# Optimization experiments

Hardware: AMD Instinct MI355X
Metric: run time of the kernel (lower is better)

The kernel has to match this reference:

```python
import jax, jax.numpy as jnp
import numpy as np

B, S, D, H = 4, 2048, 1024, 16
HD = D // H


def setup_inputs() -> dict:
    key = jax.random.key(0)
    ks = jax.random.split(key, 5)
    scale = 0.02
    return {
        "x": jax.random.normal(ks[0], (B, S, D), dtype=jnp.float32),
        "Wq": jax.random.normal(ks[1], (D, D), dtype=jnp.float32) * scale,
        "Wk": jax.random.normal(ks[2], (D, D), dtype=jnp.float32) * scale,
        "Wv": jax.random.normal(ks[3], (D, D), dtype=jnp.float32) * scale,
        "Wo": jax.random.normal(ks[4], (D, D), dtype=jnp.float32) * scale,
    }


def reference(x, Wq, Wk, Wv, Wo):
    b, s, d = x.shape
    # Linear layers (torch Linear: y = x @ W.T), no bias
    q = jnp.einsum('bsd,ed->bse', x, Wq).reshape(b, s, H, HD).transpose(0, 2, 1, 3)
    k = jnp.einsum('bsd,ed->bse', x, Wk).reshape(b, s, H, HD).transpose(0, 2, 1, 3)
    v = jnp.einsum('bsd,ed->bse', x, Wv).reshape(b, s, H, HD).transpose(0, 2, 1, 3)
    # [B,H,S,S] attention scores
    scores = jnp.einsum('bhqd,bhkd->bhqk', q, k)
    causal = jnp.tril(jnp.ones((s, s), dtype=bool))
    scores = jnp.where(causal, scores, -jnp.inf)
    # faithful to source: mask first, then scale, then softmax
    weights = jax.nn.softmax(scores / jnp.sqrt(jnp.float32(HD)), axis=-1)
    # dropout p=0.0 (eval): identity
    ctx = jnp.einsum('bhqk,bhkd->bhqd', weights, v)
    ctx = ctx.transpose(0, 2, 1, 3).reshape(b, s, d)
    return jnp.einsum('bsd,ed->bse', ctx, Wo)
```

## Files before the change

### kernel.cpp

```cpp
#include <hip/hip_runtime.h>
#include <math.h>

typedef unsigned short u16;
typedef __attribute__((ext_vector_type(8))) short short8;
typedef __attribute__((ext_vector_type(4))) float f32x4;

constexpr int Bb = 4, S_LEN = 2048, DMODEL = 1024, NH = 16;
constexpr int MTOT = Bb * S_LEN;

__device__ __forceinline__ u16 f2bf(float f) {
    union { float f; unsigned u; } v; v.f = f;
    unsigned r = v.u + 0x7FFFu + ((v.u >> 16) & 1u);
    return (u16)(r >> 16);
}

__device__ __forceinline__ void load_lds16(const void* g, void* l) {
    __builtin_amdgcn_global_load_lds(
        (const __attribute__((address_space(1))) unsigned int*)g,
        (__attribute__((address_space(3))) unsigned int*)l, 16, 0, 0);
}

__global__ __launch_bounds__(256)
void cvt_all(const float* __restrict__ x,
             const float* __restrict__ w0, const float* __restrict__ w1,
             const float* __restrict__ w2, const float* __restrict__ w3,
             u16* __restrict__ xb, u16* __restrict__ b0, u16* __restrict__ b1,
             u16* __restrict__ b2, u16* __restrict__ b3)
{
    int gid = blockIdx.x * 256 + threadIdx.x;
    constexpr int NXo = (MTOT * DMODEL) / 8;
    constexpr int NWo = (DMODEL * DMODEL) / 8;
    const float* s; u16* d; int o;
    if (gid < NXo) { s = x; d = xb; o = gid; }
    else {
        int t = gid - NXo;
        int w = t >> 17;
        o = t & (NWo - 1);
        s = (w == 0) ? w0 : (w == 1) ? w1 : (w == 2) ? w2 : w3;
        d = (w == 0) ? b0 : (w == 1) ? b1 : (w == 2) ? b2 : b3;
    }
    const float4* sp = (const float4*)(s + (size_t)o * 8);
    float4 a = sp[0], bq = sp[1];
    short8 ov;
    ov[0] = (short)f2bf(a.x);  ov[1] = (short)f2bf(a.y);
    ov[2] = (short)f2bf(a.z);  ov[3] = (short)f2bf(a.w);
    ov[4] = (short)f2bf(bq.x); ov[5] = (short)f2bf(bq.y);
    ov[6] = (short)f2bf(bq.z); ov[7] = (short)f2bf(bq.w);
    *(short8*)(d + (size_t)o * 8) = ov;
}

__global__ __launch_bounds__(256, 2)
void gemm_bt(const u16* __restrict__ X,
             const u16* __restrict__ W0, const u16* __restrict__ W1, const u16* __restrict__ W2,
             u16* __restrict__ Y0, u16* __restrict__ Y1, u16* __restrict__ Y2,
             int M, int N, int K)
{
    const u16* W = (blockIdx.z == 0) ? W0 : (blockIdx.z == 1) ? W1 : W2;
    u16*       Y = (blockIdx.z == 0) ? Y0 : (blockIdx.z == 1) ? Y1 : Y2;

    __shared__ __align__(16) u16 lA[128 * 64];
    __shared__ __align__(16) u16 lB[128 * 64];

    const int tid  = threadIdx.x;
    const int wave = tid >> 6;
    const int lane = tid & 63;
    const int qd   = lane >> 4;
    const int c    = lane & 15;
    const int tm   = blockIdx.x * 128;
    const int tn   = blockIdx.y * 128;
    const int wm   = (wave >> 1) * 64;
    const int wn   = (wave & 1) * 64;

    f32x4 acc[4][4] = {};

    for (int k0 = 0; k0 < K; k0 += 64) {
        if (k0) __syncthreads();
#pragma unroll
        for (int it = 0; it < 4; ++it) {
            int chunk = it * 256 + tid;
            int row = chunk >> 3, hc = chunk & 7;
            load_lds16(X + (size_t)(tm + row) * K + k0 + hc * 8,
                       (char*)lA + (it * 256 + wave * 64) * 16);
            load_lds16(W + (size_t)(tn + row) * K + k0 + hc * 8,
                       (char*)lB + (it * 256 + wave * 64) * 16);
        }
        __syncthreads();

#pragma unroll
        for (int kk = 0; kk < 64; kk += 32) {
            short8 a[4], b[4];
#pragma unroll
            for (int i = 0; i < 4; ++i) {
                a[i] = *(const short8*)&lA[(wm + i * 16 + c) * 64 + kk + qd * 8];
                b[i] = *(const short8*)&lB[(wn + i * 16 + c) * 64 + kk + qd * 8];
            }
#pragma unroll
            for (int mi = 0; mi < 4; ++mi)
#pragma unroll
                for (int ni = 0; ni < 4; ++ni)
                    acc[mi][ni] = __builtin_amdgcn_mfma_f32_16x16x32_bf16(
                        a[mi], b[ni], acc[mi][ni], 0, 0, 0);
        }
    }

#pragma unroll
    for (int mi = 0; mi < 4; ++mi)
#pragma unroll
        for (int ni = 0; ni < 4; ++ni)
#pragma unroll
            for (int r = 0; r < 4; ++r) {
                int row = tm + wm + mi * 16 + qd * 4 + r;
                int col = tn + wn + ni * 16 + c;
                Y[(size_t)row * N + col] = f2bf(acc[mi][ni][r]);
            }
}

__global__ __launch_bounds__(256, 2)
void gemm_bt_f32(const u16* __restrict__ X, const u16* __restrict__ W,
                 float* __restrict__ Y, int M, int N, int K)
{
    __shared__ __align__(16) u16 lA[128 * 64];
    __shared__ __align__(16) u16 lB[128 * 64];

    const int tid  = threadIdx.x;
    const int wave = tid >> 6;
    const int lane = tid & 63;
    const int qd   = lane >> 4;
    const int c    = lane & 15;
    const int tm   = blockIdx.x * 128;
    const int tn   = blockIdx.y * 128;
    const int wm   = (wave >> 1) * 64;
    const int wn   = (wave & 1) * 64;

    f32x4 acc[4][4] = {};

    for (int k0 = 0; k0 < K; k0 += 64) {
        if (k0) __syncthreads();
#pragma unroll
        for (int it = 0; it < 4; ++it) {
            int chunk = it * 256 + tid;
            int row = chunk >> 3, hc = chunk & 7;
            load_lds16(X + (size_t)(tm + row) * K + k0 + hc * 8,
                       (char*)lA + (it * 256 + wave * 64) * 16);
            load_lds16(W + (size_t)(tn + row) * K + k0 + hc * 8,
                       (char*)lB + (it * 256 + wave * 64) * 16);
        }
        __syncthreads();

#pragma unroll
        for (int kk = 0; kk < 64; kk += 32) {
            short8 a[4], b[4];
#pragma unroll
            for (int i = 0; i < 4; ++i) {
                a[i] = *(const short8*)&lA[(wm + i * 16 + c) * 64 + kk + qd * 8];
                b[i] = *(const short8*)&lB[(wn + i * 16 + c) * 64 + kk + qd * 8];
            }
#pragma unroll
            for (int mi = 0; mi < 4; ++mi)
#pragma unroll
                for (int ni = 0; ni < 4; ++ni)
                    acc[mi][ni] = __builtin_amdgcn_mfma_f32_16x16x32_bf16(
                        a[mi], b[ni], acc[mi][ni], 0, 0, 0);
        }
    }

#pragma unroll
    for (int mi = 0; mi < 4; ++mi)
#pragma unroll
        for (int ni = 0; ni < 4; ++ni)
#pragma unroll
            for (int r = 0; r < 4; ++r) {
                int row = tm + wm + mi * 16 + qd * 4 + r;
                int col = tn + wn + ni * 16 + c;
                Y[(size_t)row * N + col] = acc[mi][ni][r];
            }
}

__global__ __launch_bounds__(256)
void transpose_v(const u16* __restrict__ V, u16* __restrict__ VT)
{
    const int sblk = blockIdx.x;
    const int bh   = blockIdx.y;
    const int b = bh >> 4, h = bh & 15;
    __shared__ __align__(16) u16 lT[64][72];

    const int t = threadIdx.x;
#pragma unroll
    for (int it = 0; it < 2; ++it) {
        int chunk = it * 256 + t;
        int si = chunk >> 3, hc = chunk & 7;
        short8 val = *(const short8*)&V[(size_t)(b * S_LEN + sblk * 64 + si) * DMODEL + h * 64 + hc * 8];
        *(short8*)&lT[si][hc * 8] = val;
    }
    __syncthreads();
#pragma unroll
    for (int it = 0; it < 2; ++it) {
        int chunk = it * 256 + t;
        int hd = chunk >> 3, sc = chunk & 7;
        short8 o;
#pragma unroll
        for (int j = 0; j < 8; ++j) o[j] = (short)lT[sc * 8 + j][hd];
        *(short8*)&VT[(size_t)(bh * 64 + hd) * S_LEN + sblk * 64 + sc * 8] = o;
    }
}

__global__ __launch_bounds__(256, 2)
void attention(const u16* __restrict__ Q, const u16* __restrict__ K,
               const u16* __restrict__ VT, u16* __restrict__ CTX)
{
    const int p  = blockIdx.x;
    const int bh = blockIdx.y;
    const int b = bh >> 4, h = bh & 15;

    __shared__ __align__(16) u16 lK[2][64 * 64];
    __shared__ __align__(16) u16 lV[2][64 * 64];
    __shared__ __align__(16) u16 lP[128 * 72];

    const int tid = threadIdx.x, wave = tid >> 6, lane = tid & 63;
    const int qd = lane >> 4, c = lane & 15;
    const int wrow = wave * 32;
    const int srow = tid >> 3, shc = tid & 7;
    const int shcs = shc ^ (srow & 7);
    const int rx   = c & 7;
    const size_t kbase = (size_t)(b * S_LEN) * DMODEL + h * 64;
    const size_t vbase = (size_t)(bh * 64) * S_LEN;

#pragma unroll
    for (int phase = 0; phase < 2; ++phase) {
        const int qt = phase ? (15 - p) : p;
        const int q0 = qt * 128;
        const int nkv = 2 * qt + 2;

        short8 qf[2][2];
#pragma unroll
        for (int mi = 0; mi < 2; ++mi)
#pragma unroll
            for (int ks = 0; ks < 2; ++ks)
                qf[mi][ks] = *(const short8*)&Q[(size_t)(b * S_LEN + q0 + wrow + mi * 16 + c) * DMODEL
                                                + h * 64 + ks * 32 + qd * 8];

        f32x4 oacc[2][4] = {};
        float psum[2][4] = {};

        __syncthreads();
#pragma unroll
        for (int it = 0; it < 2; ++it) {
            load_lds16(K + kbase + (size_t)(it * 32 + srow) * DMODEL + shcs * 8,
                       (char*)lK[0] + (it * 256 + wave * 64) * 16);
            load_lds16(VT + vbase + (size_t)(it * 32 + srow) * S_LEN + shcs * 8,
                       (char*)lV[0] + (it * 256 + wave * 64) * 16);
        }

        for (int kt = 0; kt < nkv; ++kt) {
            const int cur = kt & 1;
            const int k0 = kt * 64;
            __syncthreads();

            if (kt + 1 < nkv) {
                const int kn = (kt + 1) * 64;
#pragma unroll
                for (int it = 0; it < 2; ++it) {
                    load_lds16(K + kbase + (size_t)(kn + it * 32 + srow) * DMODEL + shcs * 8,
                               (char*)lK[cur ^ 1] + (it * 256 + wave * 64) * 16);
                    load_lds16(VT + vbase + (size_t)(it * 32 + srow) * S_LEN + kn + shcs * 8,
                               (char*)lV[cur ^ 1] + (it * 256 + wave * 64) * 16);
                }
            }

            f32x4 sacc[2][4] = {};
#pragma unroll
            for (int ks = 0; ks < 2; ++ks) {
                short8 kf[4];
#pragma unroll
                for (int ni = 0; ni < 4; ++ni)
                    kf[ni] = *(const short8*)&lK[cur][(ni * 16 + c) * 64
                                                      + (((ks * 4 + qd) ^ rx) << 3)];
#pragma unroll
                for (int mi = 0; mi < 2; ++mi)
#pragma unroll
                    for (int ni = 0; ni < 4; ++ni)
                        sacc[mi][ni] = __builtin_amdgcn_mfma_f32_16x16x32_bf16(
                            qf[mi][ks], kf[ni], sacc[mi][ni], 0, 0, 0);
            }

            const bool need_mask = (k0 + 63 > q0);
#pragma unroll
            for (int mi = 0; mi < 2; ++mi)
#pragma unroll
                for (int ni = 0; ni < 4; ++ni)
#pragma unroll
                    for (int r = 0; r < 4; ++r) {
                        float t = sacc[mi][ni][r] * 0.125f;
                        if (need_mask) {
                            int colg = k0 + ni * 16 + c;
                            int rowg = q0 + wrow + mi * 16 + qd * 4 + r;
                            if (colg > rowg) t = -1.0e38f;
                        }
                        t = fminf(t, 60.0f);
                        float pv = __expf(t);
                        psum[mi][r] += pv;
                        lP[(wrow + mi * 16 + qd * 4 + r) * 72 + ni * 16 + c] = f2bf(pv);
                    }

            asm volatile("s_waitcnt lgkmcnt(0)" ::: "memory");

#pragma unroll
            for (int ks2 = 0; ks2 < 2; ++ks2) {
                short8 af[2], bf[4];
#pragma unroll
                for (int mi = 0; mi < 2; ++mi)
                    af[mi] = *(const short8*)&lP[(wrow + mi * 16 + c) * 72 + ks2 * 32 + qd * 8];
#pragma unroll
                for (int ni = 0; ni < 4; ++ni)
                    bf[ni] = *(const short8*)&lV[cur][(ni * 16 + c) * 64
                                                      + (((ks2 * 4 + qd) ^ rx) << 3)];
#pragma unroll
                for (int mi = 0; mi < 2; ++mi)
#pragma unroll
                    for (int ni = 0; ni < 4; ++ni)
                        oacc[mi][ni] = __builtin_amdgcn_mfma_f32_16x16x32_bf16(
                            af[mi], bf[ni], oacc[mi][ni], 0, 0, 0);
            }
        }

        float linv[2][4];
#pragma unroll
        for (int mi = 0; mi < 2; ++mi)
#pragma unroll
            for (int r = 0; r < 4; ++r) {
                float l = psum[mi][r];
#pragma unroll
                for (int d = 1; d < 16; d <<= 1) l += __shfl_xor(l, d);
                linv[mi][r] = 1.0f / l;
            }
#pragma unroll
        for (int mi = 0; mi < 2; ++mi)
#pragma unroll
            for (int ni = 0; ni < 4; ++ni)
#pragma unroll
                for (int r = 0; r < 4; ++r) {
                    int row = q0 + wrow + mi * 16 + qd * 4 + r;
                    CTX[(size_t)(b * S_LEN + row) * DMODEL + h * 64 + ni * 16 + c]
                        = f2bf(oacc[mi][ni][r] * linv[mi][r]);
                }
    }
}

extern "C" void kernel_launch(void* const* d_in, const int* in_sizes, int n_in,
                              void* d_out, int out_size, void* d_ws, size_t ws_size,
                              hipStream_t stream)
{
    const size_t MB = 1024 * 1024;
    char* ws = (char*)d_ws;
    if (ws_size < 72 * MB + 64) return;

    u16* xb  = (u16*)ws;
    u16* wb0 = (u16*)(ws + 16 * MB);
    u16* wb1 = (u16*)(ws + 18 * MB);
    u16* wb2 = (u16*)(ws + 20 * MB);
    u16* wb3 = (u16*)(ws + 22 * MB);
    u16* q   = (u16*)(ws + 24 * MB);
    u16* k   = (u16*)(ws + 40 * MB);
    u16* v   = (u16*)(ws + 56 * MB);
    u16* vt  = xb;
    u16* ctx = v;
    float* out = (float*)d_out;

    constexpr int NCVT = (MTOT * DMODEL + 4 * DMODEL * DMODEL) / 8 / 256;

    cvt_all<<<NCVT, 256, 0, stream>>>(
        (const float*)d_in[0], (const float*)d_in[1], (const float*)d_in[2],
        (const float*)d_in[3], (const float*)d_in[4], xb, wb0, wb1, wb2, wb3);

    gemm_bt<<<dim3(MTOT / 128, DMODEL / 128, 3), 256, 0, stream>>>(
        xb, wb0, wb1, wb2, q, k, v, MTOT, DMODEL, DMODEL);
    transpose_v<<<dim3(S_LEN / 64, Bb * NH), 256, 0, stream>>>(v, vt);
    attention<<<dim3(8, Bb * NH), 256, 0, stream>>>(q, k, vt, ctx);
    gemm_bt_f32<<<dim3(MTOT / 128, DMODEL / 128, 1), 256, 0, stream>>>(
        ctx, wb3, out, MTOT, DMODEL, DMODEL);
}
```

Before: 271.5 us.

## Split attention work across 8 waves with 16 query rows each

The attention kernel now launches 512 threads per block instead of 256, so each wave owns 16 query rows instead of 32. The K/V tile loads are spread across twice as many threads, halving each thread's load count. Per-thread register state (Q fragments, accumulators) is halved, and the launch bounds request four blocks per SM to raise occupancy and latency hiding. The cost is that each wave reuses every K/V fragment read from LDS for only one M-tile instead of two, doubling LDS read traffic per MFMA, and barriers now synchronise more waves.

Result: faster. 264.9 us (-2.4%).

```diff
diff --git a/kernel.cpp b/kernel.cpp
--- a/kernel.cpp
+++ b/kernel.cpp
@@ -204,7 +204,7 @@
     }
 }
 
-__global__ __launch_bounds__(256, 2)
+__global__ __launch_bounds__(512, 4)
 void attention(const u16* __restrict__ Q, const u16* __restrict__ K,
                const u16* __restrict__ VT, u16* __restrict__ CTX)
 {
@@ -218,7 +218,7 @@
 
     const int tid = threadIdx.x, wave = tid >> 6, lane = tid & 63;
     const int qd = lane >> 4, c = lane & 15;
-    const int wrow = wave * 32;
+    const int wrow = wave * 16;
     const int srow = tid >> 3, shc = tid & 7;
     const int shcs = shc ^ (srow & 7);
     const int rx   = c & 7;
@@ -231,25 +231,20 @@
         const int q0 = qt * 128;
         const int nkv = 2 * qt + 2;
 
-        short8 qf[2][2];
-#pragma unroll
-        for (int mi = 0; mi < 2; ++mi)
-#pragma unroll
-            for (int ks = 0; ks < 2; ++ks)
-                qf[mi][ks] = *(const short8*)&Q[(size_t)(b * S_LEN + q0 + wrow + mi * 16 + c) * DMODEL
-                                                + h * 64 + ks * 32 + qd * 8];
-
-        f32x4 oacc[2][4] = {};
-        float psum[2][4] = {};
+        short8 qf[2];
+#pragma unroll
+        for (int ks = 0; ks < 2; ++ks)
+            qf[ks] = *(const short8*)&Q[(size_t)(b * S_LEN + q0 + wrow + c) * DMODEL
+                                        + h * 64 + ks * 32 + qd * 8];
+
+        f32x4 oacc[4] = {};
+        float psum[4] = {};
 
         __syncthreads();
-#pragma unroll
-        for (int it = 0; it < 2; ++it) {
-            load_lds16(K + kbase + (size_t)(it * 32 + srow) * DMODEL + shcs * 8,
-                       (char*)lK[0] + (it * 256 + wave * 64) * 16);
-            load_lds16(VT + vbase + (size_t)(it * 32 + srow) * S_LEN + shcs * 8,
-                       (char*)lV[0] + (it * 256 + wave * 64) * 16);
-        }
+        load_lds16(K + kbase + (size_t)srow * DMODEL + shcs * 8,
+                   (char*)lK[0] + wave * 1024);
+        load_lds16(VT + vbase + (size_t)srow * S_LEN + shcs * 8,
+                   (char*)lV[0] + wave * 1024);
 
         for (int kt = 0; kt < nkv; ++kt) {
             const int cur = kt & 1;
@@ -258,16 +253,13 @@
 
             if (kt + 1 < nkv) {
                 const int kn = (kt + 1) * 64;
-#pragma unroll
-                for (int it = 0; it < 2; ++it) {
-                    load_lds16(K + kbase + (size_t)(kn + it * 32 + srow) * DMODEL + shcs * 8,
-                               (char*)lK[cur ^ 1] + (it * 256 + wave * 64) * 16);
-                    load_lds16(VT + vbase + (size_t)(it * 32 + srow) * S_LEN + kn + shcs * 8,
-                               (char*)lV[cur ^ 1] + (it * 256 + wave * 64) * 16);
-                }
-            }
-
-            f32x4 sacc[2][4] = {};
+                load_lds16(K + kbase + (size_t)(kn + srow) * DMODEL + shcs * 8,
+                           (char*)lK[cur ^ 1] + wave * 1024);
+                load_lds16(VT + vbase + (size_t)srow * S_LEN + kn + shcs * 8,
+                           (char*)lV[cur ^ 1] + wave * 1024);
+            }
+
+            f32x4 sacc[4] = {};
 #pragma unroll
             for (int ks = 0; ks < 2; ++ks) {
                 short8 kf[4];
@@ -276,73 +268,61 @@
                     kf[ni] = *(const short8*)&lK[cur][(ni * 16 + c) * 64
                                                       + (((ks * 4 + qd) ^ rx) << 3)];
 #pragma unroll
-                for (int mi = 0; mi < 2; ++mi)
-#pragma unroll
-                    for (int ni = 0; ni < 4; ++ni)
-                        sacc[mi][ni] = __builtin_amdgcn_mfma_f32_16x16x32_bf16(
-                            qf[mi][ks], kf[ni], sacc[mi][ni], 0, 0, 0);
+                for (int ni = 0; ni < 4; ++ni)
+                    sacc[ni] = __builtin_amdgcn_mfma_f32_16x16x32_bf16(
+                        qf[ks], kf[ni], sacc[ni], 0, 0, 0);
             }
 
             const bool need_mask = (k0 + 63 > q0);
 #pragma unroll
-            for (int mi = 0; mi < 2; ++mi)
-#pragma unroll
-                for (int ni = 0; ni < 4; ++ni)
-#pragma unroll
-                    for (int r = 0; r < 4; ++r) {
-                        float t = sacc[mi][ni][r] * 0.125f;
-                        if (need_mask) {
-                            int colg = k0 + ni * 16 + c;
-                            int rowg = q0 + wrow + mi * 16 + qd * 4 + r;
-                            if (colg > rowg) t = -1.0e38f;
-                        }
-                        t = fminf(t, 60.0f);
-                        float pv = __expf(t);
-                        psum[mi][r] += pv;
-                        lP[(wrow + mi * 16 + qd * 4 + r) * 72 + ni * 16 + c] = f2bf(pv);
+            for (int ni = 0; ni < 4; ++ni)
+#pragma unroll
+                for (int r = 0; r < 4; ++r) {
+                    float t = sacc[ni][r] * 0.125f;
+                    if (need_mask) {
+                        int colg = k0 + ni * 16 + c;
+                        int rowg = q0 + wrow + qd * 4 + r;
+                        if (colg > rowg) t = -1.0e38f;
                     }
+                    t = fminf(t, 60.0f);
+                    float pv = __expf(t);
+                    psum[r] += pv;
+                    lP[(wrow + qd * 4 + r) * 72 + ni * 16 + c] = f2bf(pv);
+                }
 
             asm volatile("s_waitcnt lgkmcnt(0)" ::: "memory");
 
 #pragma unroll
             for (int ks2 = 0; ks2 < 2; ++ks2) {
-                short8 af[2], bf[4];
-#pragma unroll
-                for (int mi = 0; mi < 2; ++mi)
-                    af[mi] = *(const short8*)&lP[(wrow + mi * 16 + c) * 72 + ks2 * 32 + qd * 8];
+                short8 af, bf[4];
+                af = *(const short8*)&lP[(wrow + c) * 72 + ks2 * 32 + qd * 8];
 #pragma unroll
                 for (int ni = 0; ni < 4; ++ni)
                     bf[ni] = *(const short8*)&lV[cur][(ni * 16 + c) * 64
                                                       + (((ks2 * 4 + qd) ^ rx) << 3)];
 #pragma unroll
-                for (int mi = 0; mi < 2; ++mi)
-#pragma unroll
-                    for (int ni = 0; ni < 4; ++ni)
-                        oacc[mi][ni] = __builtin_amdgcn_mfma_f32_16x16x32_bf16(
-                            af[mi], bf[ni], oacc[mi][ni], 0, 0, 0);
-            }
-        }
-
-        float linv[2][4];
-#pragma unroll
-        for (int mi = 0; mi < 2; ++mi)
+                for (int ni = 0; ni < 4; ++ni)
+                    oacc[ni] = __builtin_amdgcn_mfma_f32_16x16x32_bf16(
+                        af, bf[ni], oacc[ni], 0, 0, 0);
+            }
+        }
+
+        float linv[4];
+#pragma unroll
+        for (int r = 0; r < 4; ++r) {
+            float l = psum[r];
+#pragma unroll
+            for (int d = 1; d < 16; d <<= 1) l += __shfl_xor(l, d);
+            linv[r] = 1.0f / l;
+        }
+#pragma unroll
+        for (int ni = 0; ni < 4; ++ni)
 #pragma unroll
             for (int r = 0; r < 4; ++r) {
-                float l = psum[mi][r];
-#pragma unroll
-                for (int d = 1; d < 16; d <<= 1) l += __shfl_xor(l, d);
-                linv[mi][r] = 1.0f / l;
-            }
-#pragma unroll
-        for (int mi = 0; mi < 2; ++mi)
-#pragma unroll
-            for (int ni = 0; ni < 4; ++ni)
-#pragma unroll
-                for (int r = 0; r < 4; ++r) {
-                    int row = q0 + wrow + mi * 16 + qd * 4 + r;
-                    CTX[(size_t)(b * S_LEN + row) * DMODEL + h * 64 + ni * 16 + c]
-                        = f2bf(oacc[mi][ni][r] * linv[mi][r]);
-                }
+                int row = q0 + wrow + qd * 4 + r;
+                CTX[(size_t)(b * S_LEN + row) * DMODEL + h * 64 + ni * 16 + c]
+                    = f2bf(oacc[ni][r] * linv[r]);
+            }
     }
 }
 
@@ -375,7 +355,7 @@
     gemm_bt<<<dim3(MTOT / 128, DMODEL / 128, 3), 256, 0, stream>>>(
         xb, wb0, wb1, wb2, q, k, v, MTOT, DMODEL, DMODEL);
     transpose_v<<<dim3(S_LEN / 64, Bb * NH), 256, 0, stream>>>(v, vt);
-    attention<<<dim3(8, Bb * NH), 256, 0, stream>>>(q, k, vt, ctx);
+    attention<<<dim3(8, Bb * NH), 512, 0, stream>>>(q, k, vt, ctx);
     gemm_bt_f32<<<dim3(MTOT / 128, DMODEL / 128, 1), 256, 0, stream>>>(
         ctx, wb3, out, MTOT, DMODEL, DMODEL);
 }
```
